# Kernel optimization log

Measured on AMD Instinct MI355X. Metric: run time of the kernel, lower is better.

The kernel has to match this reference:

```python
import jax, jax.numpy as jnp
import numpy as np

DIM = 1024
HEADS = 16


def setup_inputs() -> dict:
    key = jax.random.key(0)
    ks = jax.random.split(key, 9)
    B, N, C = 2, 2048, DIM
    hd = C // HEADS
    s = 1.0 / np.sqrt(C)
    x = jax.random.normal(ks[0], (B, N, C), dtype=jnp.float32)
    wq = jax.random.normal(ks[1], (C, C), dtype=jnp.float32) * s
    wk = jax.random.normal(ks[2], (C, C), dtype=jnp.float32) * s
    wv = jax.random.normal(ks[3], (C, C), dtype=jnp.float32) * s
    wp = jax.random.normal(ks[4], (C, C), dtype=jnp.float32) * s
    bp = jnp.zeros((C,), dtype=jnp.float32)
    # rotary table: angles theta_j = 10000^{-2j/hd}, positions 0..N-1
    inv_freq = 1.0 / (10000.0 ** (jnp.arange(0, hd, 2, dtype=jnp.float32) / hd))
    ang = jnp.arange(N, dtype=jnp.float32)[:, None] * inv_freq[None, :]  # (N, hd//2)
    cos = jnp.cos(ang)
    sin = jnp.sin(ang)
    return {"x": x, "wq": wq, "wk": wk, "wv": wv, "wp": wp, "bp": bp,
            "cos": cos, "sin": sin, "num_heads": HEADS}


def _apply_rotary(t, cos, sin):
    # t: (B, N, H, D); cos/sin: (N, D//2) -> broadcast (1, N, 1, D//2)
    B, N, H, D = t.shape
    tr = t.reshape(B, N, H, D // 2, 2)
    t1, t2 = tr[..., 0], tr[..., 1]
    c = cos[None, :, None, :]
    s = sin[None, :, None, :]
    o1 = t1 * c - t2 * s
    o2 = t1 * s + t2 * c
    return jnp.stack([o1, o2], axis=-1).reshape(B, N, H, D)


def reference(x, wq, wk, wv, wp, bp, cos, sin, num_heads):
    B, N, C = x.shape
    H = num_heads
    D = C // H
    q = (x @ wq.T).reshape(B, N, H, D)
    k = (x @ wk.T).reshape(B, N, H, D)
    v = (x @ wv.T).reshape(B, N, H, D)
    q = _apply_rotary(q, cos, sin)
    k = _apply_rotary(k, cos, sin)
    scale = 1.0 / jnp.sqrt(jnp.asarray(D, dtype=x.dtype))
    # scores: (B, H, N, N)
    scores = jnp.einsum('bnhd,bmhd->bhnm', q, k) * scale
    attn = jax.nn.softmax(scores, axis=-1)
    out = jnp.einsum('bhnm,bmhd->bnhd', attn, v).reshape(B, N, C)
    return out @ wp.T + bp
```

## Files before the change

### kernel.cpp

```cpp
#include <hip/hip_runtime.h>
#include <hip/hip_bf16.h>
#include <stdint.h>

#define DEVI __device__ __forceinline__

using bf16 = __hip_bfloat16;
typedef __bf16 bf16x8 __attribute__((ext_vector_type(8)));
typedef float f32x4 __attribute__((ext_vector_type(4)));

static constexpr int Bb = 2, Nn = 2048, Cc = 1024, Hh = 16, Dd = 64;
static constexpr float CSC = 0.125f * 1.44269504088896340736f;

DEVI bf16 f2bf(float x) {
  __bf16 h = (__bf16)x;
  return *(bf16*)&h;
}
DEVI float fexp2(float x) { return __builtin_amdgcn_exp2f(x); }

DEVI bf16x8 cvt8(f32x4 a, f32x4 b) {
  bf16x8 r;
  r[0] = (__bf16)a[0]; r[1] = (__bf16)a[1]; r[2] = (__bf16)a[2]; r[3] = (__bf16)a[3];
  r[4] = (__bf16)b[0]; r[5] = (__bf16)b[1]; r[6] = (__bf16)b[2]; r[7] = (__bf16)b[3];
  return r;
}

DEVI void gld_lds16(const bf16* g, bf16* l) {
  __builtin_amdgcn_global_load_lds(
      (__attribute__((address_space(1))) void*)(g),
      (__attribute__((address_space(3))) void*)(l),
      16, 0, 0);
}

__global__ __launch_bounds__(256) void k_cvt(const float* __restrict__ x,
                                             const float* __restrict__ wq,
                                             const float* __restrict__ wk,
                                             const float* __restrict__ wv,
                                             const float* __restrict__ wp,
                                             bf16* xb, bf16* wqb, bf16* wkb,
                                             bf16* wvb, bf16* wpb) {
  int bid = blockIdx.x;
  const float* src; bf16* dst; size_t off;
  if (bid < 2048) {
    src = x; dst = xb; off = (size_t)bid * 2048;
  } else {
    int s = (bid - 2048) >> 9, r = (bid - 2048) & 511;
    off = (size_t)r * 2048;
    src = s == 0 ? wq : s == 1 ? wk : s == 2 ? wv : wp;
    dst = s == 0 ? wqb : s == 1 ? wkb : s == 2 ? wvb : wpb;
  }
  size_t i = off + (size_t)threadIdx.x * 8;
  f32x4 a = *(const f32x4*)(src + i);
  f32x4 b = *(const f32x4*)(src + i + 4);
  *(bf16x8*)(dst + i) = cvt8(a, b);
}

template <int MFC, class Epi>
DEVI void gemm_lds_body(const bf16* __restrict__ A, const bf16* __restrict__ Bw,
                        int K, int m0, int n0, bf16* lA, bf16* lB, Epi epi) {
  constexpr int BM = MFC * 32;
  constexpr int PA = BM / 64;
  const int t = threadIdx.x;
  const int lane = t & 63, wave = t >> 6;
  const int wr = wave >> 1, wc = wave & 1;

  f32x4 acc[MFC][4] = {};

  for (int k0 = 0; k0 < K; k0 += 32) {
    __syncthreads();
#pragma unroll
    for (int p = 0; p < PA; ++p) {
      int c = p * 256 + t;
      int row = c >> 2, col = (c & 3) * 8;
      gld_lds16(A + (size_t)(m0 + row) * K + k0 + col,
                lA + (size_t)(p * 256 + wave * 64) * 8);
    }
#pragma unroll
    for (int p = 0; p < 2; ++p) {
      int c = p * 256 + t;
      int row = c >> 2, col = (c & 3) * 8;
      gld_lds16(Bw + (size_t)(n0 + row) * K + k0 + col,
                lB + (size_t)(p * 256 + wave * 64) * 8);
    }
    __syncthreads();

    bf16x8 aF[MFC];
#pragma unroll
    for (int mf = 0; mf < MFC; ++mf)
      aF[mf] = *(const bf16x8*)(lA + (wr * (BM / 2) + mf * 16 + (lane & 15)) * 32 + (lane >> 4) * 8);
#pragma unroll
    for (int nf = 0; nf < 4; ++nf) {
      bf16x8 bF = *(const bf16x8*)(lB + (wc * 64 + nf * 16 + (lane & 15)) * 32 + (lane >> 4) * 8);
#pragma unroll
      for (int mf = 0; mf < MFC; ++mf)
        acc[mf][nf] = __builtin_amdgcn_mfma_f32_16x16x32_bf16(aF[mf], bF, acc[mf][nf], 0, 0, 0);
    }
  }

#pragma unroll
  for (int mf = 0; mf < MFC; ++mf)
#pragma unroll
    for (int nf = 0; nf < 4; ++nf)
#pragma unroll
      for (int r = 0; r < 4; ++r) {
        int gm = m0 + wr * (BM / 2) + mf * 16 + (lane >> 4) * 4 + r;
        int gn = n0 + wc * 64 + nf * 16 + (lane & 15);
        epi(gm, gn, acc[mf][nf][r]);
      }
}

struct EpiRope {
  bf16* dst; const float* cosw; const float* sinw; float scale;
  DEVI void operator()(int gm, int gn, float v) const {
    int b = gm >> 11, n = gm & 2047;
    int h = gn >> 6, d = gn & 63;
    int i = d >> 1;
    float c = cosw[n * 32 + i], s = sinw[n * 32 + i];
    float p = __shfl_xor(v, 1);
    float o = (d & 1) ? (p * s + v * c) : (v * c - p * s);
    dst[((size_t)(b * Hh + h) * Nn + n) * 64 + d] = f2bf(o * scale);
  }
};

struct EpiVt {
  bf16* dst;
  DEVI void operator()(int gm, int gn, float v) const {
    int h = gm >> 6, d = gm & 63;
    int b = gn >> 11, n = gn & 2047;
    dst[((size_t)(b * Hh + h) * 64 + d) * Nn + n] = f2bf(v);
  }
};

struct EpiProj {
  float* dst; const float* bias;
  DEVI void operator()(int gm, int gn, float v) const {
    dst[(size_t)gm * Cc + gn] = v + bias[gn];
  }
};

__global__ __launch_bounds__(256) void k_qkv(const bf16* __restrict__ xb,
                                             const bf16* __restrict__ wqb,
                                             const bf16* __restrict__ wkb,
                                             const bf16* __restrict__ wvb,
                                             bf16* q_ws, bf16* k_ws, bf16* vt_ws,
                                             const float* __restrict__ cw,
                                             const float* __restrict__ sw) {
  __shared__ __align__(16) bf16 smem[256 * 32];
  bf16* lA = smem;
  bf16* lB = smem + 128 * 32;
  int bid = blockIdx.x;
  if (bid < 512) {
    int sub = bid & 255;
    int m0 = (sub >> 3) * 128, n0 = (sub & 7) * 128;
    bool isq = bid < 256;
    gemm_lds_body<4>(xb, isq ? wqb : wkb, Cc, m0, n0, lA, lB,
                     EpiRope{isq ? q_ws : k_ws, cw, sw, isq ? CSC : 1.0f});
  } else {
    int sub = bid - 512;
    int m0 = (sub & 7) * 128, n0 = (sub >> 3) * 128;
    gemm_lds_body<4>(wvb, xb, Cc, m0, n0, lA, lB, EpiVt{vt_ws});
  }
}

__global__ __launch_bounds__(256) void k_proj(const bf16* __restrict__ A,
                                              const bf16* __restrict__ W,
                                              float* dst, const float* __restrict__ bias) {
  __shared__ __align__(16) bf16 smem[192 * 32];
  gemm_lds_body<2>(A, W, Cc, blockIdx.x * 64, blockIdx.y * 128,
                   smem, smem + 64 * 32, EpiProj{dst, bias});
}

__global__ __launch_bounds__(256) void k_flash(const bf16* __restrict__ q_ws,
                                               const bf16* __restrict__ k_ws,
                                               const bf16* __restrict__ vt_ws,
                                               bf16* __restrict__ attn_o) {
  __shared__ __align__(16) bf16 lK[2][64 * 64];
  __shared__ __align__(16) bf16 lV[2][64 * 64];
  __shared__ __align__(16) bf16 pbuf[4][32 * 64];

  const int t = threadIdx.x, lane = t & 63, wave = t >> 6;
  const int bh = blockIdx.y;
  const int q0 = blockIdx.x * 128 + wave * 32;
  const bf16* qg = q_ws + (size_t)bh * Nn * 64;
  const bf16* kg = k_ws + (size_t)bh * Nn * 64;
  const bf16* vg = vt_ws + (size_t)bh * 64 * Nn;

  bf16x8 qF[2][2];
#pragma unroll
  for (int qs = 0; qs < 2; ++qs)
#pragma unroll
    for (int kd = 0; kd < 2; ++kd)
      qF[qs][kd] = *(const bf16x8*)(qg + (size_t)(q0 + qs * 16 + (lane & 15)) * 64 + kd * 32 + (lane >> 4) * 8);

  f32x4 accO[2][4] = {};
  float LsL[2][4] = {};

  bf16x8 rk[2], rv[2];
  auto load_tile = [&](int kt) {
#pragma unroll
    for (int p = 0; p < 2; ++p) {
      int c = p * 256 + t;
      int row = c >> 3, col = (c & 7) * 8;
      rk[p] = *(const bf16x8*)(kg + (size_t)(kt * 64 + row) * 64 + col);
      rv[p] = *(const bf16x8*)(vg + (size_t)row * Nn + kt * 64 + col);
    }
  };
  auto store_tile = [&](int buf) {
#pragma unroll
    for (int p = 0; p < 2; ++p) {
      int c = p * 256 + t;
      int row = c >> 3;
      int idx = (row * 64 + (c & 7) * 8) ^ ((row & 7) << 3);
      *(bf16x8*)(lK[buf] + idx) = rk[p];
      *(bf16x8*)(lV[buf] + idx) = rv[p];
    }
  };

  load_tile(0);
  store_tile(0);
  __syncthreads();

  constexpr int NT = Nn / 64;
  for (int kt = 0; kt < NT; ++kt) {
    const int cur = kt & 1;
    if (kt + 1 < NT) load_tile(kt + 1);

    f32x4 accS[2][4];
#pragma unroll
    for (int nf = 0; nf < 4; ++nf) {
      int row = nf * 16 + (lane & 15);
      int i0 = (row * 64 + 0 * 32 + (lane >> 4) * 8) ^ ((row & 7) << 3);
      int i1 = (row * 64 + 1 * 32 + (lane >> 4) * 8) ^ ((row & 7) << 3);
      bf16x8 kF0 = *(const bf16x8*)(lK[cur] + i0);
      bf16x8 kF1 = *(const bf16x8*)(lK[cur] + i1);
#pragma unroll
      for (int qs = 0; qs < 2; ++qs) {
        f32x4 sacc = {};
        sacc = __builtin_amdgcn_mfma_f32_16x16x32_bf16(qF[qs][0], kF0, sacc, 0, 0, 0);
        sacc = __builtin_amdgcn_mfma_f32_16x16x32_bf16(qF[qs][1], kF1, sacc, 0, 0, 0);
        accS[qs][nf] = sacc;
      }
    }

#pragma unroll
    for (int qs = 0; qs < 2; ++qs)
#pragma unroll
      for (int nf = 0; nf < 4; ++nf)
#pragma unroll
        for (int r = 0; r < 4; ++r) {
          float pv = fexp2(accS[qs][nf][r]);
          LsL[qs][r] += pv;
          int prow = qs * 16 + (lane >> 4) * 4 + r;
          int pidx = (prow * 64 + nf * 16 + (lane & 15)) ^ ((prow & 7) << 3);
          pbuf[wave][pidx] = f2bf(pv);
        }

#pragma unroll
    for (int kd = 0; kd < 2; ++kd) {
      bf16x8 pF[2];
#pragma unroll
      for (int qs = 0; qs < 2; ++qs) {
        int prow = qs * 16 + (lane & 15);
        int pidx = (prow * 64 + kd * 32 + (lane >> 4) * 8) ^ ((prow & 7) << 3);
        pF[qs] = *(const bf16x8*)(&pbuf[wave][pidx]);
      }
#pragma unroll
      for (int nf = 0; nf < 4; ++nf) {
        int row = nf * 16 + (lane & 15);
        int iv = (row * 64 + kd * 32 + (lane >> 4) * 8) ^ ((row & 7) << 3);
        bf16x8 vF = *(const bf16x8*)(lV[cur] + iv);
#pragma unroll
        for (int qs = 0; qs < 2; ++qs)
          accO[qs][nf] = __builtin_amdgcn_mfma_f32_16x16x32_bf16(pF[qs], vF, accO[qs][nf], 0, 0, 0);
      }
    }

    if (kt + 1 < NT) store_tile(cur ^ 1);
    __syncthreads();
  }

  const int b = bh >> 4, h = bh & 15;
#pragma unroll
  for (int qs = 0; qs < 2; ++qs)
#pragma unroll
    for (int r = 0; r < 4; ++r) {
      float s = LsL[qs][r];
      s += __shfl_xor(s, 1);
      s += __shfl_xor(s, 2);
      s += __shfl_xor(s, 4);
      s += __shfl_xor(s, 8);
      float inv = 1.0f / s;
      int qrow = q0 + qs * 16 + (lane >> 4) * 4 + r;
#pragma unroll
      for (int nf = 0; nf < 4; ++nf) {
        int d = nf * 16 + (lane & 15);
        attn_o[((size_t)(b * Nn + qrow)) * Cc + h * 64 + d] = f2bf(accO[qs][nf][r] * inv);
      }
    }
}

extern "C" void kernel_launch(void* const* d_in, const int* in_sizes, int n_in,
                              void* d_out, int out_size, void* d_ws, size_t ws_size,
                              hipStream_t stream) {
  (void)in_sizes; (void)n_in; (void)out_size; (void)ws_size;
  const float* x  = (const float*)d_in[0];
  const float* wq = (const float*)d_in[1];
  const float* wk = (const float*)d_in[2];
  const float* wv = (const float*)d_in[3];
  const float* wp = (const float*)d_in[4];
  const float* bp = (const float*)d_in[5];
  const float* cw = (const float*)d_in[6];
  const float* sw = (const float*)d_in[7];
  float* out = (float*)d_out;

  const size_t M1 = 1u << 20;
  bf16* x_bf  = (bf16*)d_ws;
  bf16* wq_bf = x_bf + 4 * M1;
  bf16* wk_bf = wq_bf + M1;
  bf16* wv_bf = wk_bf + M1;
  bf16* wp_bf = wv_bf + M1;
  bf16* q_ws  = wp_bf + M1;
  bf16* k_ws  = q_ws + 4 * M1;
  bf16* vt_ws = k_ws + 4 * M1;
  bf16* ao_ws = x_bf;

  k_cvt  <<<dim3(4096),    dim3(256), 0, stream>>>(x, wq, wk, wv, wp,
                                                   x_bf, wq_bf, wk_bf, wv_bf, wp_bf);
  k_qkv  <<<dim3(768),     dim3(256), 0, stream>>>(x_bf, wq_bf, wk_bf, wv_bf,
                                                   q_ws, k_ws, vt_ws, cw, sw);
  k_flash<<<dim3(16, 32),  dim3(256), 0, stream>>>(q_ws, k_ws, vt_ws, ao_ws);
  k_proj <<<dim3(64, 8),   dim3(256), 0, stream>>>(ao_ws, wp_bf, out, bp);
}
```

Measured before the change: 131.1 us.

## Widen GEMM K-tile with swizzled LDS and stage flash tiles via direct loads

The GEMM main loop now covers 64 of K per iteration instead of 32, with an XOR-swizzled LDS layout to avoid bank conflicts, which halves the number of barriers. The flash kernel stages K/V tiles straight from global memory into LDS with direct global-to-LDS loads instead of going through registers. It also computes S transposed so that P can be written to LDS as packed 4-element stores, with a cheaper row-sum reduction. It adds s_setprio around the MFMA phases. The costs are more LDS per block, which may lower occupancy, and the risk that the direct prefetch into the other buffer races with reads still in flight.

```diff
diff --git a/kernel.cpp b/kernel.cpp
--- a/kernel.cpp
+++ b/kernel.cpp
@@ -6,6 +6,7 @@
 
 using bf16 = __hip_bfloat16;
 typedef __bf16 bf16x8 __attribute__((ext_vector_type(8)));
+typedef __bf16 bf16x4 __attribute__((ext_vector_type(4)));
 typedef float f32x4 __attribute__((ext_vector_type(4)));
 
 static constexpr int Bb = 2, Nn = 2048, Cc = 1024, Hh = 16, Dd = 64;
@@ -58,41 +59,47 @@
 DEVI void gemm_lds_body(const bf16* __restrict__ A, const bf16* __restrict__ Bw,
                         int K, int m0, int n0, bf16* lA, bf16* lB, Epi epi) {
   constexpr int BM = MFC * 32;
-  constexpr int PA = BM / 64;
+  constexpr int PA = BM / 32;
   const int t = threadIdx.x;
   const int lane = t & 63, wave = t >> 6;
   const int wr = wave >> 1, wc = wave & 1;
 
   f32x4 acc[MFC][4] = {};
 
-  for (int k0 = 0; k0 < K; k0 += 32) {
+  for (int k0 = 0; k0 < K; k0 += 64) {
     __syncthreads();
 #pragma unroll
     for (int p = 0; p < PA; ++p) {
       int c = p * 256 + t;
-      int row = c >> 2, col = (c & 3) * 8;
-      gld_lds16(A + (size_t)(m0 + row) * K + k0 + col,
+      int row = c >> 3, cis = (c & 7) ^ (row & 7);
+      gld_lds16(A + (size_t)(m0 + row) * K + k0 + cis * 8,
                 lA + (size_t)(p * 256 + wave * 64) * 8);
     }
 #pragma unroll
-    for (int p = 0; p < 2; ++p) {
+    for (int p = 0; p < 4; ++p) {
       int c = p * 256 + t;
-      int row = c >> 2, col = (c & 3) * 8;
-      gld_lds16(Bw + (size_t)(n0 + row) * K + k0 + col,
+      int row = c >> 3, cis = (c & 7) ^ (row & 7);
+      gld_lds16(Bw + (size_t)(n0 + row) * K + k0 + cis * 8,
                 lB + (size_t)(p * 256 + wave * 64) * 8);
     }
     __syncthreads();
 
-    bf16x8 aF[MFC];
-#pragma unroll
-    for (int mf = 0; mf < MFC; ++mf)
-      aF[mf] = *(const bf16x8*)(lA + (wr * (BM / 2) + mf * 16 + (lane & 15)) * 32 + (lane >> 4) * 8);
-#pragma unroll
-    for (int nf = 0; nf < 4; ++nf) {
-      bf16x8 bF = *(const bf16x8*)(lB + (wc * 64 + nf * 16 + (lane & 15)) * 32 + (lane >> 4) * 8);
-#pragma unroll
-      for (int mf = 0; mf < MFC; ++mf)
-        acc[mf][nf] = __builtin_amdgcn_mfma_f32_16x16x32_bf16(aF[mf], bF, acc[mf][nf], 0, 0, 0);
+#pragma unroll
+    for (int kk = 0; kk < 2; ++kk) {
+      bf16x8 aF[MFC];
+#pragma unroll
+      for (int mf = 0; mf < MFC; ++mf) {
+        int row = wr * (BM / 2) + mf * 16 + (lane & 15);
+        aF[mf] = *(const bf16x8*)(lA + ((row * 64 + kk * 32 + (lane >> 4) * 8) ^ ((row & 7) << 3)));
+      }
+#pragma unroll
+      for (int nf = 0; nf < 4; ++nf) {
+        int row = wc * 64 + nf * 16 + (lane & 15);
+        bf16x8 bF = *(const bf16x8*)(lB + ((row * 64 + kk * 32 + (lane >> 4) * 8) ^ ((row & 7) << 3)));
+#pragma unroll
+        for (int mf = 0; mf < MFC; ++mf)
+          acc[mf][nf] = __builtin_amdgcn_mfma_f32_16x16x32_bf16(aF[mf], bF, acc[mf][nf], 0, 0, 0);
+      }
     }
   }
 
@@ -144,9 +151,9 @@
                                              bf16* q_ws, bf16* k_ws, bf16* vt_ws,
                                              const float* __restrict__ cw,
                                              const float* __restrict__ sw) {
-  __shared__ __align__(16) bf16 smem[256 * 32];
+  __shared__ __align__(16) bf16 smem[2 * 128 * 64];
   bf16* lA = smem;
-  bf16* lB = smem + 128 * 32;
+  bf16* lB = smem + 128 * 64;
   int bid = blockIdx.x;
   if (bid < 512) {
     int sub = bid & 255;
@@ -164,9 +171,9 @@
 __global__ __launch_bounds__(256) void k_proj(const bf16* __restrict__ A,
                                               const bf16* __restrict__ W,
                                               float* dst, const float* __restrict__ bias) {
-  __shared__ __align__(16) bf16 smem[192 * 32];
+  __shared__ __align__(16) bf16 smem[64 * 64 + 128 * 64];
   gemm_lds_body<2>(A, W, Cc, blockIdx.x * 64, blockIdx.y * 128,
-                   smem, smem + 64 * 32, EpiProj{dst, bias});
+                   smem, smem + 64 * 64, EpiProj{dst, bias});
 }
 
 __global__ __launch_bounds__(256) void k_flash(const bf16* __restrict__ q_ws,
@@ -178,6 +185,7 @@
   __shared__ __align__(16) bf16 pbuf[4][32 * 64];
 
   const int t = threadIdx.x, lane = t & 63, wave = t >> 6;
+  const int g = lane >> 4;
   const int bh = blockIdx.y;
   const int q0 = blockIdx.x * 128 + wave * 32;
   const bf16* qg = q_ws + (size_t)bh * Nn * 64;
@@ -189,107 +197,108 @@
   for (int qs = 0; qs < 2; ++qs)
 #pragma unroll
     for (int kd = 0; kd < 2; ++kd)
-      qF[qs][kd] = *(const bf16x8*)(qg + (size_t)(q0 + qs * 16 + (lane & 15)) * 64 + kd * 32 + (lane >> 4) * 8);
+      qF[qs][kd] = *(const bf16x8*)(qg + (size_t)(q0 + qs * 16 + (lane & 15)) * 64 + kd * 32 + g * 8);
 
   f32x4 accO[2][4] = {};
-  float LsL[2][4] = {};
-
-  bf16x8 rk[2], rv[2];
-  auto load_tile = [&](int kt) {
+  float LsL[2] = {0.f, 0.f};
+
+  auto stage_tile = [&](int kt, int buf) {
 #pragma unroll
     for (int p = 0; p < 2; ++p) {
       int c = p * 256 + t;
-      int row = c >> 3, col = (c & 7) * 8;
-      rk[p] = *(const bf16x8*)(kg + (size_t)(kt * 64 + row) * 64 + col);
-      rv[p] = *(const bf16x8*)(vg + (size_t)row * Nn + kt * 64 + col);
+      int row = c >> 3, cis = (c & 7) ^ (row & 7);
+      bf16* dst = (bf16*)((p * 256 + wave * 64) * 8);
+      gld_lds16(kg + (size_t)(kt * 64 + row) * 64 + cis * 8,
+                lK[buf] + (size_t)(p * 256 + wave * 64) * 8);
+      gld_lds16(vg + (size_t)row * Nn + kt * 64 + cis * 8,
+                lV[buf] + (size_t)(p * 256 + wave * 64) * 8);
+      (void)dst;
     }
   };
-  auto store_tile = [&](int buf) {
-#pragma unroll
-    for (int p = 0; p < 2; ++p) {
-      int c = p * 256 + t;
-      int row = c >> 3;
-      int idx = (row * 64 + (c & 7) * 8) ^ ((row & 7) << 3);
-      *(bf16x8*)(lK[buf] + idx) = rk[p];
-      *(bf16x8*)(lV[buf] + idx) = rv[p];
-    }
-  };
-
-  load_tile(0);
-  store_tile(0);
+
+  stage_tile(0, 0);
   __syncthreads();
 
   constexpr int NT = Nn / 64;
   for (int kt = 0; kt < NT; ++kt) {
     const int cur = kt & 1;
-    if (kt + 1 < NT) load_tile(kt + 1);
-
-    f32x4 accS[2][4];
+    if (kt + 1 < NT) stage_tile(kt + 1, cur ^ 1);
+
+    f32x4 accT[2][4];
+    __builtin_amdgcn_s_setprio(1);
 #pragma unroll
     for (int nf = 0; nf < 4; ++nf) {
       int row = nf * 16 + (lane & 15);
-      int i0 = (row * 64 + 0 * 32 + (lane >> 4) * 8) ^ ((row & 7) << 3);
-      int i1 = (row * 64 + 1 * 32 + (lane >> 4) * 8) ^ ((row & 7) << 3);
-      bf16x8 kF0 = *(const bf16x8*)(lK[cur] + i0);
-      bf16x8 kF1 = *(const bf16x8*)(lK[cur] + i1);
+      bf16x8 kF0 = *(const bf16x8*)(lK[cur] + ((row * 64 + 0 * 32 + g * 8) ^ ((row & 7) << 3)));
+      bf16x8 kF1 = *(const bf16x8*)(lK[cur] + ((row * 64 + 1 * 32 + g * 8) ^ ((row & 7) << 3)));
 #pragma unroll
       for (int qs = 0; qs < 2; ++qs) {
         f32x4 sacc = {};
-        sacc = __builtin_amdgcn_mfma_f32_16x16x32_bf16(qF[qs][0], kF0, sacc, 0, 0, 0);
-        sacc = __builtin_amdgcn_mfma_f32_16x16x32_bf16(qF[qs][1], kF1, sacc, 0, 0, 0);
-        accS[qs][nf] = sacc;
-      }
-    }
-
-#pragma unroll
-    for (int qs = 0; qs < 2; ++qs)
-#pragma unroll
-      for (int nf = 0; nf < 4; ++nf)
+        sacc = __builtin_amdgcn_mfma_f32_16x16x32_bf16(kF0, qF[qs][0], sacc, 0, 0, 0);
+        sacc = __builtin_amdgcn_mfma_f32_16x16x32_bf16(kF1, qF[qs][1], sacc, 0, 0, 0);
+        accT[qs][nf] = sacc;
+      }
+    }
+    __builtin_amdgcn_s_setprio(0);
+
+#pragma unroll
+    for (int qs = 0; qs < 2; ++qs) {
+      int prow = qs * 16 + (lane & 15);
+      float ps = 0.f;
+#pragma unroll
+      for (int nf = 0; nf < 4; ++nf) {
+        bf16x4 pk;
 #pragma unroll
         for (int r = 0; r < 4; ++r) {
-          float pv = fexp2(accS[qs][nf][r]);
-          LsL[qs][r] += pv;
-          int prow = qs * 16 + (lane >> 4) * 4 + r;
-          int pidx = (prow * 64 + nf * 16 + (lane & 15)) ^ ((prow & 7) << 3);
-          pbuf[wave][pidx] = f2bf(pv);
+          float pv = fexp2(accT[qs][nf][r]);
+          ps += pv;
+          pk[r] = (__bf16)pv;
         }
-
+        int idx = (prow * 64 + nf * 16 + g * 4) ^ ((prow & 7) << 3);
+        *(bf16x4*)(pbuf[wave] + idx) = pk;
+      }
+      LsL[qs] += ps;
+    }
+
+    __builtin_amdgcn_s_setprio(1);
 #pragma unroll
     for (int kd = 0; kd < 2; ++kd) {
       bf16x8 pF[2];
 #pragma unroll
       for (int qs = 0; qs < 2; ++qs) {
         int prow = qs * 16 + (lane & 15);
-        int pidx = (prow * 64 + kd * 32 + (lane >> 4) * 8) ^ ((prow & 7) << 3);
-        pF[qs] = *(const bf16x8*)(&pbuf[wave][pidx]);
+        pF[qs] = *(const bf16x8*)(pbuf[wave] + ((prow * 64 + kd * 32 + g * 8) ^ ((prow & 7) << 3)));
       }
 #pragma unroll
       for (int nf = 0; nf < 4; ++nf) {
         int row = nf * 16 + (lane & 15);
-        int iv = (row * 64 + kd * 32 + (lane >> 4) * 8) ^ ((row & 7) << 3);
-        bf16x8 vF = *(const bf16x8*)(lV[cur] + iv);
+        bf16x8 vF = *(const bf16x8*)(lV[cur] + ((row * 64 + kd * 32 + g * 8) ^ ((row & 7) << 3)));
 #pragma unroll
         for (int qs = 0; qs < 2; ++qs)
           accO[qs][nf] = __builtin_amdgcn_mfma_f32_16x16x32_bf16(pF[qs], vF, accO[qs][nf], 0, 0, 0);
       }
     }
-
-    if (kt + 1 < NT) store_tile(cur ^ 1);
+    __builtin_amdgcn_s_setprio(0);
+
     __syncthreads();
   }
 
+  float Lq[2];
+#pragma unroll
+  for (int qs = 0; qs < 2; ++qs) {
+    float s = LsL[qs];
+    s += __shfl_xor(s, 16);
+    s += __shfl_xor(s, 32);
+    Lq[qs] = s;
+  }
+
   const int b = bh >> 4, h = bh & 15;
 #pragma unroll
   for (int qs = 0; qs < 2; ++qs)
 #pragma unroll
     for (int r = 0; r < 4; ++r) {
-      float s = LsL[qs][r];
-      s += __shfl_xor(s, 1);
-      s += __shfl_xor(s, 2);
-      s += __shfl_xor(s, 4);
-      s += __shfl_xor(s, 8);
-      float inv = 1.0f / s;
-      int qrow = q0 + qs * 16 + (lane >> 4) * 4 + r;
+      float inv = 1.0f / __shfl(Lq[qs], g * 4 + r);
+      int qrow = q0 + qs * 16 + g * 4 + r;
 #pragma unroll
       for (int nf = 0; nf < 4; ++nf) {
         int d = nf * 16 + (lane & 15);
```

Result: slower. 134.2 us (+2.3%).
